# Kernel tuning notes

Measured on AMD Instinct MI355X. Metric: run time of the kernel, lower is better.

## Reference

```python
import jax, jax.numpy as jnp
import numpy as np

N = 30000
E = 480000
D_IN = 128
EPS = 1e-5
NEG_SLOPE = 0.2
# (in_dim, out_channels, heads) per GATConv layer; concat=True everywhere (PyG default)
CFG = [(D_IN, 100, 5), (500, 50, 5), (250, 32, 4), (128, 8, 4), (32, 1, 1)]
BN_DIMS = (500, 250, 128)


def setup_inputs() -> dict:
    key = jax.random.key(0)
    ks = iter(jax.random.split(key, 80))
    inp = {
        "x": jax.random.normal(next(ks), (N, D_IN), jnp.float32),
        "edge_index": jax.random.randint(next(ks), (2, E), 0, N),
        "edge_weight": jax.random.uniform(next(ks), (E, 1), jnp.float32),
    }
    for l, (cin, cout, h) in enumerate(CFG, 1):
        s = 1.0 / np.sqrt(cin)
        inp[f"W{l}"] = jax.random.normal(next(ks), (cin, h * cout), jnp.float32) * s
        inp[f"a_s{l}"] = jax.random.normal(next(ks), (1, h, cout), jnp.float32) * 0.1
        inp[f"a_d{l}"] = jax.random.normal(next(ks), (1, h, cout), jnp.float32) * 0.1
        inp[f"We{l}"] = jax.random.normal(next(ks), (1, h * cout), jnp.float32)
        inp[f"a_e{l}"] = jax.random.normal(next(ks), (1, h, cout), jnp.float32) * 0.1
        inp[f"b{l}"] = jnp.zeros((h * cout,), jnp.float32)
    for l, d in zip((1, 2, 3), BN_DIMS):
        inp[f"g{l}"] = jnp.ones((d,), jnp.float32)
        inp[f"beta{l}"] = jnp.zeros((d,), jnp.float32)
    return inp


def _gat(x, src, dst, ea, W, a_s, a_d, We, a_e, b, heads, cout):
    """PyG GATConv with edge_dim attention (concat=True)."""
    n = x.shape[0]
    h = (x @ W).reshape(n, heads, cout)            # [N,H,C]
    e = (ea @ We).reshape(-1, heads, cout)         # [E,H,C]
    al_src = (h * a_s).sum(-1)                     # [N,H]
    al_dst = (h * a_d).sum(-1)                     # [N,H]
    logit = jax.nn.leaky_relu(al_src[src] + al_dst[dst] + (e * a_e).sum(-1), NEG_SLOPE)
    m = jax.ops.segment_max(logit, dst, num_segments=n)
    m = jnp.where(jnp.isfinite(m), m, 0.0)
    ex = jnp.exp(logit - m[dst])                   # [E,H]
    den = jax.ops.segment_sum(ex, dst, num_segments=n)
    alpha = ex / jnp.maximum(den[dst], 1e-16)      # segment softmax over in-edges of dst
    out = jax.ops.segment_sum(h[src] * alpha[..., None], dst, num_segments=n)
    return out.reshape(n, heads * cout) + b


def _bn(x, g, b):
    mu = x.mean(0)
    var = x.var(0)  # biased, as torch uses for normalization
    return (x - mu) * jax.lax.rsqrt(var + EPS) * g + b


def reference(x, edge_index, edge_weight,
              W1, a_s1, a_d1, We1, a_e1, b1,
              W2, a_s2, a_d2, We2, a_e2, b2,
              W3, a_s3, a_d3, We3, a_e3, b3,
              W4, a_s4, a_d4, We4, a_e4, b4,
              W5, a_s5, a_d5, We5, a_e5, b5,
              g1, beta1, g2, beta2, g3, beta3):
    # add self loops (PyG default) with edge_attr fill_value='mean'
    loop = jnp.arange(N)
    src = jnp.concatenate([edge_index[0], loop])
    dst = jnp.concatenate([edge_index[1], loop])
    ea = jnp.concatenate([edge_weight, jnp.full((N, 1), edge_weight.mean(), edge_weight.dtype)], axis=0)

    h = _gat(x, src, dst, ea, W1, a_s1, a_d1, We1, a_e1, b1, 5, 100)
    h = jax.nn.relu(_bn(h, g1, beta1))
    h = _gat(h, src, dst, ea, W2, a_s2, a_d2, We2, a_e2, b2, 5, 50)
    h = jax.nn.relu(_bn(h, g2, beta2))
    h = _gat(h, src, dst, ea, W3, a_s3, a_d3, We3, a_e3, b3, 4, 32)
    h = jax.nn.relu(_bn(h, g3, beta3))
    h = _gat(h, src, dst, ea, W4, a_s4, a_d4, We4, a_e4, b4, 4, 8)
    h = jax.nn.relu(h)
    h = _gat(h, src, dst, ea, W5, a_s5, a_d5, We5, a_e5, b5, 1, 1)
    return h
```

## Files before the change

### kernel.cpp

```cpp
#include <hip/hip_runtime.h>
#include <hip/hip_bf16.h>
#include <math.h>

#define NN 30000
#define EE 480000
#define ET (EE + NN)
#define NEG_SLOPE 0.2f
#define BN_EPS 1e-5f

struct LayerCfg { int cin, C, H; };
static const LayerCfg g_cfg[5] = {
    {128, 100, 5}, {500, 50, 5}, {250, 32, 4}, {128, 8, 4}, {32, 1, 1}
};

typedef short short8 __attribute__((ext_vector_type(8)));
typedef float f32x4 __attribute__((ext_vector_type(4)));

__device__ __forceinline__ unsigned short f2bf(float f) {
    unsigned int u = __builtin_bit_cast(unsigned int, f);
    u = (u + 0x7FFFu + ((u >> 16) & 1u)) >> 16;
    return (unsigned short)u;
}
__device__ __forceinline__ float bf2f(unsigned short h) {
    unsigned int u = ((unsigned int)h) << 16;
    return __builtin_bit_cast(float, u);
}


struct PrepArgs {
    const float* W[5];
    const float* We[5];
    const float* ae[5];
    unsigned short* bh[5];
    unsigned short* bl[5];
    float* wedot;
    int K[5], N[5], Kp[5], Np[5], C[5], H[5];
};

static const int EBLK = (ET + 255) / 256;

__global__ void prep_fused_kernel(const int* __restrict__ ei, int* __restrict__ rank,
                                  int* __restrict__ cnt, const float* __restrict__ ew,
                                  float* __restrict__ esum, PrepArgs a) {
    __shared__ float sdata[256];
    __shared__ float tile[32][33];
    int b = blockIdx.x;
    int tid = threadIdx.x;

    if (b < EBLK) {
        int e = b * 256 + tid;
        if (e < ET) {
            int d = (e < EE) ? ei[EE + e] : (e - EE);
            rank[e] = atomicAdd(&cnt[d], 1);
        }
        return;
    }
    b -= EBLK;
    if (b < 256) {
        float s = 0.f;
        for (int i = b * 256 + tid; i < EE; i += 65536)
            s += ew[i];
        sdata[tid] = s;
        __syncthreads();
        for (int off = 128; off > 0; off >>= 1) {
            if (tid < off) sdata[tid] += sdata[tid + off];
            __syncthreads();
        }
        if (tid == 0) atomicAdd(esum, sdata[0]);
        return;
    }
    b -= 256;
    int bx = b & 15, by = (b >> 4) & 15, bz = b >> 8;
    int l = bz;
    int tx = tid & 31, ty = tid >> 5;
    if (bx == 0 && by == 0 && ty == 0 && tx < 8) {
        int hd = tx;
        if (hd < a.H[l]) {
            int C = a.C[l];
            const float* We = a.We[l] + hd * C;
            const float* ae = a.ae[l] + hd * C;
            float s = 0.f;
            for (int c = 0; c < C; c++) s += We[c] * ae[c];
            a.wedot[l * 8 + hd] = s;
        }
    }
    int Kp = a.Kp[l], Np = a.Np[l], K = a.K[l], N = a.N[l];
    int kb = bx * 32, nb = by * 32;
    if (kb >= Kp || nb >= Np) return;
    const float* B = a.W[l];
    unsigned short* Bth = a.bh[l];
    unsigned short* Btl = a.bl[l];
#pragma unroll
    for (int i = 0; i < 4; i++) {
        int k = kb + ty + i * 8, n = nb + tx;
        tile[ty + i * 8][tx] = (k < K && n < N) ? B[(size_t)k * N + n] : 0.f;
    }
    __syncthreads();
#pragma unroll
    for (int i = 0; i < 4; i++) {
        int n = nb + ty + i * 8, k = kb + tx;
        if (n < Np && k < Kp) {
            float v = tile[tx][ty + i * 8];
            unsigned short hi = f2bf(v);
            unsigned short lo = f2bf(v - bf2f(hi));
            size_t idx = (size_t)n * Kp + k;
            Bth[idx] = hi;
            Btl[idx] = lo;
        }
    }
}

__global__ void scan_kernel(const int* __restrict__ cnt, int* __restrict__ off) {
    __shared__ int lsum[1024];
    const int T = 1024;
    int t = threadIdx.x;
    int chunk = (NN + T - 1) / T;
    int base = t * chunk;
    int end = min(NN, base + chunk);
    int s = 0;
    for (int i = base; i < end; i++) s += cnt[i];
    lsum[t] = s;
    __syncthreads();
    for (int d = 1; d < T; d <<= 1) {
        int v = (t >= d) ? lsum[t - d] : 0;
        __syncthreads();
        lsum[t] += v;
        __syncthreads();
    }
    int run = (t == 0) ? 0 : lsum[t - 1];
    for (int i = base; i < end; i++) {
        off[i] = run;
        run += cnt[i];
    }
    if (t == 0) off[NN] = ET;
}

__global__ void fill_kernel(const int* __restrict__ ei, const int* __restrict__ rank,
                            const float* __restrict__ ew, const float* __restrict__ esum,
                            const int* __restrict__ off,
                            int* __restrict__ csr_src, float* __restrict__ csr_ea) {
    int e = blockIdx.x * blockDim.x + threadIdx.x;
    if (e >= ET) return;
    int sv, d;
    if (e < EE) { sv = ei[e]; d = ei[EE + e]; }
    else        { sv = e - EE; d = e - EE; }
    int p = off[d] + rank[e];
    csr_src[p] = sv;
    csr_ea[p]  = (e < EE) ? ew[e] : esum[0] * (1.0f / (float)EE);
}

#define GBM 128
#define GBNT 128
#define GBK 32
#define ASTR 36
__global__ __launch_bounds__(256) void gemm_split_kernel(const float* __restrict__ A,
                                                         const unsigned short* __restrict__ Bt_hi,
                                                         const unsigned short* __restrict__ Bt_lo,
                                                         float* __restrict__ Cm,
                                                         unsigned short* __restrict__ Ch16,
                                                         int M, int Kp, int Nc,
                                                         const float* __restrict__ colsum,
                                                         const float* __restrict__ colsumsq,
                                                         const float* __restrict__ g,
                                                         const float* __restrict__ beta,
                                                         int D) {
    __shared__ short AsH[GBM * ASTR];
    __shared__ short AsL[GBM * ASTR];
    __shared__ short BsH[GBNT * ASTR];
    __shared__ short BsL[GBNT * ASTR];
    __shared__ float sscale[512];
    __shared__ float sshift[512];
    int tid = threadIdx.x;
    bool bn = (colsum != nullptr);
    if (bn) {
        for (int c = tid; c < Kp; c += 256) {
            float sc = 0.f, sh = 0.f;
            if (c < D) {
                float mu = colsum[c] * (1.0f / (float)NN);
                float var = colsumsq[c] * (1.0f / (float)NN) - mu * mu;
                sc = g[c] * rsqrtf(var + BN_EPS);
                sh = beta[c] - mu * sc;
            }
            sscale[c] = sc;
            sshift[c] = sh;
        }
        __syncthreads();
    }
    int wave = tid >> 6, lane = tid & 63;
    int q = lane >> 4, r = lane & 15;
    int m0 = blockIdx.y * GBM, n0 = blockIdx.x * GBNT;
    int wm = (wave & 1) * 64, wn = (wave >> 1) * 64;
    f32x4 acc[4][4];
#pragma unroll
    for (int i = 0; i < 4; i++)
#pragma unroll
        for (int j = 0; j < 4; j++) acc[i][j] = (f32x4)(0.f);

    int arow2 = tid >> 1;
    int acol2 = (tid & 1) * 16;
    int brow = tid >> 2;
    int bcol = (tid & 3) * 8;

    int ksteps = Kp / GBK;
    for (int ks = 0; ks < ksteps; ks++) {
        int k0 = ks * GBK;
        {
            int m = m0 + arow2;
            float v[16];
            if (m < M) {
                const float* Ap = A + (size_t)m * Kp + k0 + acol2;
                float4 f0 = *(const float4*)(Ap);
                float4 f1 = *(const float4*)(Ap + 4);
                float4 f2 = *(const float4*)(Ap + 8);
                float4 f3 = *(const float4*)(Ap + 12);
                v[0]=f0.x; v[1]=f0.y; v[2]=f0.z; v[3]=f0.w;
                v[4]=f1.x; v[5]=f1.y; v[6]=f1.z; v[7]=f1.w;
                v[8]=f2.x; v[9]=f2.y; v[10]=f2.z; v[11]=f2.w;
                v[12]=f3.x; v[13]=f3.y; v[14]=f3.z; v[15]=f3.w;
                if (bn) {
                    int cb = k0 + acol2;
#pragma unroll
                    for (int i = 0; i < 16; i++)
                        v[i] = fmaxf(v[i] * sscale[cb + i] + sshift[cb + i], 0.f);
                }
            } else {
#pragma unroll
                for (int i = 0; i < 16; i++) v[i] = 0.f;
            }
#pragma unroll
            for (int i = 0; i < 16; i++) {
                unsigned short hi = f2bf(v[i]);
                unsigned short lo = f2bf(v[i] - bf2f(hi));
                AsH[arow2 * ASTR + acol2 + i] = (short)hi;
                AsL[arow2 * ASTR + acol2 + i] = (short)lo;
            }
        }
#pragma unroll
        for (int p = 0; p < 2; p++) {
            int row = p * 64 + brow;
            size_t gidx = (size_t)(n0 + row) * Kp + k0 + bcol;
            *((uint4*)(BsH + row * ASTR + bcol)) = *((const uint4*)(Bt_hi + gidx));
            *((uint4*)(BsL + row * ASTR + bcol)) = *((const uint4*)(Bt_lo + gidx));
        }
        __syncthreads();
        short8 ah[4], al[4], bh[4], bl[4];
#pragma unroll
        for (int i = 0; i < 4; i++) {
            ah[i] = *((const short8*)(AsH + (wm + i * 16 + r) * ASTR + q * 8));
            al[i] = *((const short8*)(AsL + (wm + i * 16 + r) * ASTR + q * 8));
        }
#pragma unroll
        for (int j = 0; j < 4; j++) {
            bh[j] = *((const short8*)(BsH + (wn + j * 16 + r) * ASTR + q * 8));
            bl[j] = *((const short8*)(BsL + (wn + j * 16 + r) * ASTR + q * 8));
        }
#pragma unroll
        for (int i = 0; i < 4; i++)
#pragma unroll
            for (int j = 0; j < 4; j++) {
                acc[i][j] = __builtin_amdgcn_mfma_f32_16x16x32_bf16(ah[i], bh[j], acc[i][j], 0, 0, 0);
                acc[i][j] = __builtin_amdgcn_mfma_f32_16x16x32_bf16(ah[i], bl[j], acc[i][j], 0, 0, 0);
                acc[i][j] = __builtin_amdgcn_mfma_f32_16x16x32_bf16(al[i], bh[j], acc[i][j], 0, 0, 0);
            }
        __syncthreads();
    }
#pragma unroll
    for (int i = 0; i < 4; i++) {
#pragma unroll
        for (int j = 0; j < 4; j++) {
#pragma unroll
            for (int reg = 0; reg < 4; reg++) {
                int mrow = m0 + wm + i * 16 + q * 4 + reg;
                int ncol = n0 + wn + j * 16 + r;
                if (mrow < M && ncol < Nc) {
                    float val = acc[i][j][reg];
                    if (Cm)   Cm[(size_t)mrow * Nc + ncol] = val;
                    if (Ch16) Ch16[(size_t)mrow * Nc + ncol] = f2bf(val);
                }
            }
        }
    }
}

__global__ void gemv_l5_kernel(const float* __restrict__ X, const float* __restrict__ W,
                               const float* __restrict__ a_s, const float* __restrict__ a_d,
                               float* __restrict__ h, float* __restrict__ al_src,
                               float* __restrict__ al_dst) {
    __shared__ float w[32];
    if (threadIdx.x < 32) w[threadIdx.x] = W[threadIdx.x];
    __syncthreads();
    int n = blockIdx.x * blockDim.x + threadIdx.x;
    if (n >= NN) return;
    const float* row = X + (size_t)n * 32;
    float s = 0.f;
#pragma unroll
    for (int i = 0; i < 8; i++) {
        float4 f = *(const float4*)(row + i * 4);
        s += f.x * w[i * 4] + f.y * w[i * 4 + 1] + f.z * w[i * 4 + 2] + f.w * w[i * 4 + 3];
    }
    h[n] = s;
    al_src[n] = s * a_s[0];
    al_dst[n] = s * a_d[0];
}

__global__ void al_wave_h16_kernel(const unsigned short* __restrict__ h16,
                                   const float* __restrict__ a_s,
                                   const float* __restrict__ a_d,
                                   float* __restrict__ al_src, float* __restrict__ al_dst,
                                   int H, int C, int HCp) {
    int w = (blockIdx.x * blockDim.x + threadIdx.x) >> 6;
    int lane = threadIdx.x & 63;
    if (w >= NN) return;
    const unsigned short* row = h16 + (size_t)w * HCp;
    float s1[5] = {0.f, 0.f, 0.f, 0.f, 0.f};
    float s2[5] = {0.f, 0.f, 0.f, 0.f, 0.f};
#pragma unroll
    for (int hd = 0; hd < 5; hd++) {
        if (hd >= H) break;
        int base = hd * C;
        for (int c = lane * 2; c < C; c += 128) {
            unsigned int u = *(const unsigned int*)(row + base + c);
            float v0 = bf2f((unsigned short)(u & 0xffffu));
            float v1 = bf2f((unsigned short)(u >> 16));
            s1[hd] += v0 * a_s[base + c] + v1 * a_s[base + c + 1];
            s2[hd] += v0 * a_d[base + c] + v1 * a_d[base + c + 1];
        }
    }
#pragma unroll
    for (int hd = 0; hd < 5; hd++) {
        if (hd >= H) break;
#pragma unroll
        for (int off = 32; off > 0; off >>= 1) {
            s1[hd] += __shfl_xor(s1[hd], off, 64);
            s2[hd] += __shfl_xor(s2[hd], off, 64);
        }
    }
    if (lane == 0) {
#pragma unroll
        for (int hd = 0; hd < 5; hd++) {
            if (hd >= H) break;
            al_src[(size_t)w * H + hd] = s1[hd];
            al_dst[(size_t)w * H + hd] = s2[hd];
        }
    }
}

__global__ void attn_kernel(const float* __restrict__ al_src,
                            const float* __restrict__ al_dst,
                            const int* __restrict__ csr_src,
                            const float* __restrict__ csr_ea,
                            const float* __restrict__ we_dot,
                            const int* __restrict__ off,
                            float* __restrict__ alpha_t, int H, int NH) {
    int t = blockIdx.x * blockDim.x + threadIdx.x;
    if (t >= NH) return;
    int n = t / H, hd = t - n * H;
    int s = off[n], e = off[n + 1];
    float ad = al_dst[(size_t)n * H + hd];
    float wd = we_dot[hd];
    float* arow = alpha_t + (size_t)hd * ET;
    float m = -INFINITY, l = 0.f;
    int p = s;
    for (; p + 3 < e; p += 4) {
        int s0 = csr_src[p], s1 = csr_src[p + 1], s2 = csr_src[p + 2], s3 = csr_src[p + 3];
        float w0 = csr_ea[p], w1 = csr_ea[p + 1], w2 = csr_ea[p + 2], w3 = csr_ea[p + 3];
        float l0 = al_src[(size_t)s0 * H + hd] + ad + w0 * wd;
        float l1 = al_src[(size_t)s1 * H + hd] + ad + w1 * wd;
        float l2 = al_src[(size_t)s2 * H + hd] + ad + w2 * wd;
        float l3 = al_src[(size_t)s3 * H + hd] + ad + w3 * wd;
        l0 = (l0 >= 0.f) ? l0 : NEG_SLOPE * l0;
        l1 = (l1 >= 0.f) ? l1 : NEG_SLOPE * l1;
        l2 = (l2 >= 0.f) ? l2 : NEG_SLOPE * l2;
        l3 = (l3 >= 0.f) ? l3 : NEG_SLOPE * l3;
        arow[p] = l0; arow[p + 1] = l1; arow[p + 2] = l2; arow[p + 3] = l3;
        float mq = fmaxf(fmaxf(l0, l1), fmaxf(l2, l3));
        float nm = fmaxf(m, mq);
        l = l * __expf(m - nm)
          + __expf(l0 - nm) + __expf(l1 - nm) + __expf(l2 - nm) + __expf(l3 - nm);
        m = nm;
    }
    for (; p < e; p++) {
        float lg = al_src[(size_t)csr_src[p] * H + hd] + ad + csr_ea[p] * wd;
        lg = (lg >= 0.f) ? lg : NEG_SLOPE * lg;
        arow[p] = lg;
        float nm = fmaxf(m, lg);
        l = l * __expf(m - nm) + __expf(lg - nm);
        m = nm;
    }
    float inv = 1.f / fmaxf(l, 1e-16f);
    for (p = s; p < e; p++) arow[p] = __expf(arow[p] - m) * inv;
}

__global__ void aggregate_slab_kernel(const unsigned short* __restrict__ h16,
                                      const float* __restrict__ alpha_t,
                                      const int* __restrict__ off,
                                      const int* __restrict__ csr_src,
                                      const float* __restrict__ bias,
                                      float* __restrict__ out,
                                      int C, int H, int HC, int hp,
                                      int lns, int lcps, int npr,
                                      int relu, int opitch) {
    int vs = blockIdx.x & 7;
    int nb = blockIdx.x >> 3;
    int slab = vs & ((1 << lns) - 1);
    int rep  = vs >> lns;
    int tid = threadIdx.x;
    int cps = 1 << lcps;
    int lc = tid & (cps - 1);
    int ln = tid >> lcps;
    int npb = 256 >> lcps;
    int nl = nb * npb + ln;
    if (nl >= npr) return;
    int n = rep * npr + nl;
    int j = (slab << (lcps + 2)) + (lc << 2);

    int hdA = j / C;
    int hdB = (j + 3) / C;
    int bnd = (hdA + 1) * C - j;
    bnd = (bnd > 4) ? 4 : bnd;
    float mA = (hdA < H) ? 1.f : 0.f;
    float mB = (hdB < H) ? 1.f : 0.f;
    const float* arA = alpha_t + (size_t)((hdA < H) ? hdA : 0) * ET;
    const float* arB = alpha_t + (size_t)((hdB < H) ? hdB : 0) * ET;

    int s = off[n], e = off[n + 1];
    const unsigned short* hb = h16 + j;
    float ac0 = 0.f, ac1 = 0.f, ac2 = 0.f, ac3 = 0.f;
    int p = s;
    for (; p + 3 < e; p += 4) {
        int idx[4]; float aA[4], aB[4];
#pragma unroll
        for (int u = 0; u < 4; u++) {
            idx[u] = csr_src[p + u];
            aA[u] = arA[p + u];
            aB[u] = arB[p + u];
        }
#pragma unroll
        for (int u = 0; u < 4; u++) {
            ushort4 uv = *(const ushort4*)(hb + (size_t)idx[u] * hp);
            ac0 += ((0 < bnd) ? aA[u] : aB[u]) * bf2f(uv.x);
            ac1 += ((1 < bnd) ? aA[u] : aB[u]) * bf2f(uv.y);
            ac2 += ((2 < bnd) ? aA[u] : aB[u]) * bf2f(uv.z);
            ac3 += ((3 < bnd) ? aA[u] : aB[u]) * bf2f(uv.w);
        }
    }
    for (; p < e; p++) {
        int i0 = csr_src[p];
        float aA0 = arA[p], aB0 = arB[p];
        ushort4 uv = *(const ushort4*)(hb + (size_t)i0 * hp);
        ac0 += ((0 < bnd) ? aA0 : aB0) * bf2f(uv.x);
        ac1 += ((1 < bnd) ? aA0 : aB0) * bf2f(uv.y);
        ac2 += ((2 < bnd) ? aA0 : aB0) * bf2f(uv.z);
        ac3 += ((3 < bnd) ? aA0 : aB0) * bf2f(uv.w);
    }
    float o0 = ac0 * ((0 < bnd) ? mA : mB) + ((j + 0 < HC) ? bias[j + 0] : 0.f);
    float o1 = ac1 * ((1 < bnd) ? mA : mB) + ((j + 1 < HC) ? bias[j + 1] : 0.f);
    float o2 = ac2 * ((2 < bnd) ? mA : mB) + ((j + 2 < HC) ? bias[j + 2] : 0.f);
    float o3 = ac3 * ((3 < bnd) ? mA : mB) + ((j + 3 < HC) ? bias[j + 3] : 0.f);
    if (relu) {
        o0 = fmaxf(o0, 0.f); o1 = fmaxf(o1, 0.f);
        o2 = fmaxf(o2, 0.f); o3 = fmaxf(o3, 0.f);
    }
    *(float4*)(out + (size_t)n * opitch + j) = make_float4(o0, o1, o2, o3);
}

__global__ void aggregate_kernel(const float* __restrict__ hfeat,
                                 const float* __restrict__ alpha_t,
                                 const int* __restrict__ off, const int* __restrict__ csr_src,
                                 const float* __restrict__ bias, float* __restrict__ out,
                                 int total) {
    int t = blockIdx.x * blockDim.x + threadIdx.x;
    if (t >= total) return;
    int n = t;
    int s = off[n], e = off[n + 1];
    float acc = 0.f;
    int p = s;
    for (; p + 3 < e; p += 4) {
        acc += alpha_t[p] * hfeat[csr_src[p]]
             + alpha_t[p + 1] * hfeat[csr_src[p + 1]]
             + alpha_t[p + 2] * hfeat[csr_src[p + 2]]
             + alpha_t[p + 3] * hfeat[csr_src[p + 3]];
    }
    for (; p < e; p++) acc += alpha_t[p] * hfeat[csr_src[p]];
    out[n] = acc + bias[0];
}


__global__ void bn_stats_kernel(const float* __restrict__ x, float* __restrict__ colsum,
                                float* __restrict__ colsumsq, int D, int pitch) {
    int rows_per_block = (NN + gridDim.x - 1) / gridDim.x;
    int r0 = blockIdx.x * rows_per_block;
    int r1 = min(NN, r0 + rows_per_block);
    int c0 = threadIdx.x;
    int c1 = threadIdx.x + 256;
    float s0 = 0.f, q0 = 0.f, s1 = 0.f, q1 = 0.f;
    for (int r = r0; r < r1; r++) {
        const float* row = x + (size_t)r * pitch;
        if (c0 < D) { float v = row[c0]; s0 += v; q0 += v * v; }
        if (c1 < D) { float v = row[c1]; s1 += v; q1 += v * v; }
    }
    if (c0 < D) { atomicAdd(&colsum[c0], s0); atomicAdd(&colsumsq[c0], q0); }
    if (c1 < D) { atomicAdd(&colsum[c1], s1); atomicAdd(&colsumsq[c1], q1); }
}


static inline size_t align_up(size_t v, size_t a) { return (v + a - 1) / a * a; }

extern "C" void kernel_launch(void* const* d_in, const int* in_sizes, int n_in,
                              void* d_out, int out_size, void* d_ws, size_t ws_size,
                              hipStream_t stream) {
    const float* x_in = (const float*)d_in[0];
    const int* ei     = (const int*)d_in[1];
    const float* ew   = (const float*)d_in[2];

    char* pws = (char*)d_ws;
    size_t off_b = 0;
    auto alloc = [&](size_t bytes) -> void* {
        void* rp = pws + off_b;
        off_b = align_up(off_b + bytes, 256);
        return rp;
    };
    float* B0      = (float*)alloc((size_t)NN * 4);
    float* B1      = (float*)alloc((size_t)NN * 512 * 4);
    unsigned short* H16 = (unsigned short*)alloc((size_t)NN * 512 * 2);
    float* alpha_t = (float*)alloc((size_t)ET * 5 * 4);
    unsigned short* Wt_hi = (unsigned short*)alloc((size_t)600 * 512 * 2);
    unsigned short* Wt_lo = (unsigned short*)alloc((size_t)600 * 512 * 2);
    float* al_src  = (float*)alloc((size_t)NN * 5 * 4);
    float* al_dst  = (float*)alloc((size_t)NN * 5 * 4);
    float* csr_ea  = (float*)alloc((size_t)ET * 4);
    int* rankb     = (int*)alloc((size_t)ET * 4);
    int* csr_src   = (int*)alloc((size_t)ET * 4);
    int* offarr    = (int*)alloc((size_t)(NN + 1) * 4);
    float* we_dot  = (float*)alloc(40 * 4);
    float* esum    = (float*)alloc(4);
    int* cnt       = (int*)alloc((size_t)NN * 4);
    float* colsum_all   = (float*)alloc(3 * 512 * 4);
    float* colsumsq_all = (float*)alloc(3 * 512 * 4);
    char* zero_end = pws + off_b;
    (void)ws_size; (void)n_in; (void)in_sizes; (void)out_size;

    int Kp[5], Np[5], hp[5];
    size_t wtoff[5];
    size_t acc_off = 0;
    for (int l = 0; l < 5; l++) {
        int K = g_cfg[l].cin, HC = g_cfg[l].C * g_cfg[l].H;
        Kp[l] = (K + 31) / 32 * 32;
        Np[l] = (HC + 127) / 128 * 128;
        hp[l] = (HC >= 64) ? ((HC + 63) / 64 * 64) : ((HC + 7) / 8 * 8);
        wtoff[l] = acc_off;
        acc_off += (size_t)Kp[l] * Np[l];
    }

    PrepArgs pa;
    for (int l = 0; l < 5; l++) {
        pa.W[l]  = (const float*)d_in[3 + l * 6 + 0];
        pa.We[l] = (const float*)d_in[3 + l * 6 + 3];
        pa.ae[l] = (const float*)d_in[3 + l * 6 + 4];
        pa.bh[l] = Wt_hi + wtoff[l];
        pa.bl[l] = Wt_lo + wtoff[l];
        pa.K[l] = g_cfg[l].cin;
        pa.N[l] = g_cfg[l].C * g_cfg[l].H;
        pa.Kp[l] = Kp[l];
        pa.Np[l] = Np[l];
        pa.C[l] = g_cfg[l].C;
        pa.H[l] = g_cfg[l].H;
    }
    pa.wedot = we_dot;

    hipMemsetAsync(esum, 0, (size_t)(zero_end - (char*)esum), stream);
    int ebl = EBLK;
    prep_fused_kernel<<<ebl + 256 + 1280, 256, 0, stream>>>(ei, rankb, cnt, ew, esum, pa);
    scan_kernel<<<1, 1024, 0, stream>>>(cnt, offarr);
    fill_kernel<<<ebl, 256, 0, stream>>>(ei, rankb, ew, esum, offarr, csr_src, csr_ea);

    for (int l = 0; l < 5; l++) {
        const LayerCfg& cf = g_cfg[l];
        int H = cf.H, C = cf.C;
        int HC = H * C;
        const float* a_s = (const float*)d_in[3 + l * 6 + 1];
        const float* a_d = (const float*)d_in[3 + l * 6 + 2];
        const float* b   = (const float*)d_in[3 + l * 6 + 5];

        const float* X = (l == 0) ? x_in : B1;
        float* outbuf = (l == 4) ? (float*)d_out : B1;
        int opitch = (l == 4) ? 1 : Kp[l + 1];
        int NH = NN * H;
        int alblocks = (NN * 64 + 255) / 256;

        if (l == 4) {
            gemv_l5_kernel<<<(NN + 255) / 256, 256, 0, stream>>>(
                X, pa.W[4], a_s, a_d, B0, al_src, al_dst);
        } else {
            const float* cs = (l >= 1) ? colsum_all + (l - 1) * 512 : nullptr;
            const float* cq = (l >= 1) ? colsumsq_all + (l - 1) * 512 : nullptr;
            const float* gg = (l >= 1) ? (const float*)d_in[33 + (l - 1) * 2 + 0] : nullptr;
            const float* bb = (l >= 1) ? (const float*)d_in[33 + (l - 1) * 2 + 1] : nullptr;
            int Din = (l >= 1) ? g_cfg[l - 1].C * g_cfg[l - 1].H : 0;
            dim3 ggrid(Np[l] / GBNT, (NN + GBM - 1) / GBM);
            gemm_split_kernel<<<ggrid, 256, 0, stream>>>(X, Wt_hi + wtoff[l], Wt_lo + wtoff[l],
                                                         nullptr, H16,
                                                         NN, Kp[l], hp[l], cs, cq, gg, bb, Din);
            al_wave_h16_kernel<<<alblocks, 256, 0, stream>>>(H16, a_s, a_d, al_src, al_dst, H, C, hp[l]);
        }

        attn_kernel<<<(NH + 255) / 256, 256, 0, stream>>>(al_src, al_dst, csr_src, csr_ea,
                                                          we_dot + l * 8, offarr, alpha_t, H, NH);

        if (l == 4) {
            aggregate_kernel<<<(NN + 255) / 256, 256, 0, stream>>>(
                B0, alpha_t, offarr, csr_src, b, outbuf, NN);
        } else {
            int cps = (hp[l] >= 64) ? 16 : 8;
            int lcps = (cps == 16) ? 4 : 3;
            int nslabs = hp[l] / (cps * 4);
            int lns = (nslabs == 8) ? 3 : (nslabs == 4) ? 2 : (nslabs == 2) ? 1 : 0;
            int dup = 8 / nslabs;
            int npr = NN / dup;
            int npb = 256 / cps;
            int gx = 8 * ((npr + npb - 1) / npb);
            aggregate_slab_kernel<<<gx, 256, 0, stream>>>(
                H16, alpha_t, offarr, csr_src, b, outbuf,
                C, H, HC, hp[l], lns, lcps, npr, (l == 3) ? 1 : 0, opitch);
        }

        if (l < 3) {
            bn_stats_kernel<<<512, 256, 0, stream>>>(outbuf, colsum_all + l * 512,
                                                     colsumsq_all + l * 512, HC, opitch);
        }
    }
}
```

Measured before the change: 821.3 us.

## Stage neighbor indices and attention weights in LDS for slab aggregation

```diff
diff --git a/kernel.cpp b/kernel.cpp
--- a/kernel.cpp
+++ b/kernel.cpp
@@ -391,72 +391,122 @@
     for (p = s; p < e; p++) arow[p] = __expf(arow[p] - m) * inv;
 }
 
-__global__ void aggregate_slab_kernel(const unsigned short* __restrict__ h16,
-                                      const float* __restrict__ alpha_t,
-                                      const int* __restrict__ off,
-                                      const int* __restrict__ csr_src,
-                                      const float* __restrict__ bias,
-                                      float* __restrict__ out,
-                                      int C, int H, int HC, int hp,
-                                      int lns, int lcps, int npr,
-                                      int relu, int opitch) {
+#define AGG_T 64
+__global__ void aggregate_slab_lds_kernel(const unsigned short* __restrict__ h16,
+                                          const float* __restrict__ alpha_t,
+                                          const int* __restrict__ off,
+                                          const int* __restrict__ csr_src,
+                                          const float* __restrict__ bias,
+                                          float* __restrict__ out,
+                                          int C, int H, int HC, int hp,
+                                          int lns, int lcps, int npr, int nhs,
+                                          int relu, int opitch) {
+    extern __shared__ char smem[];
+    int cps = 1 << lcps;
+    int G = 256 >> lcps;
+    int* sidx = (int*)smem;
+    float* sal = (float*)(smem + (size_t)G * AGG_T * 4);
+    __shared__ int s_maxt;
+
     int vs = blockIdx.x & 7;
     int nb = blockIdx.x >> 3;
     int slab = vs & ((1 << lns) - 1);
     int rep  = vs >> lns;
     int tid = threadIdx.x;
-    int cps = 1 << lcps;
     int lc = tid & (cps - 1);
-    int ln = tid >> lcps;
-    int npb = 256 >> lcps;
-    int nl = nb * npb + ln;
-    if (nl >= npr) return;
-    int n = rep * npr + nl;
-    int j = (slab << (lcps + 2)) + (lc << 2);
+    int g = tid >> lcps;
+    int nl = nb * G + g;
+    bool active = (nl < npr);
+    int n = rep * npr + (active ? nl : 0);
+
+    int slab_j = slab << (lcps + 2);
+    int j = slab_j + (lc << 2);
+    int hlo = slab_j / C;
+    int hhi = (slab_j + (cps << 2) - 1) / C;
+    if (hhi > H - 1) hhi = H - 1;
+    int nval = hhi - hlo + 1;
 
     int hdA = j / C;
     int hdB = (j + 3) / C;
     int bnd = (hdA + 1) * C - j;
     bnd = (bnd > 4) ? 4 : bnd;
-    float mA = (hdA < H) ? 1.f : 0.f;
-    float mB = (hdB < H) ? 1.f : 0.f;
-    const float* arA = alpha_t + (size_t)((hdA < H) ? hdA : 0) * ET;
-    const float* arB = alpha_t + (size_t)((hdB < H) ? hdB : 0) * ET;
-
-    int s = off[n], e = off[n + 1];
+    int selA = hdA - hlo; if (selA >= nhs) selA = nhs - 1;
+    int selB = hdB - hlo; if (selB >= nhs) selB = nhs - 1;
+
+    int s = active ? off[n] : 0;
+    int e = active ? off[n + 1] : 0;
+    int nt = (e - s + AGG_T - 1) / AGG_T;
+
+    if (tid == 0) s_maxt = 0;
+    __syncthreads();
+    if (lc == 0 && active && nt > 0) atomicMax(&s_maxt, nt);
+    __syncthreads();
+    int maxt = s_maxt;
+
     const unsigned short* hb = h16 + j;
+    int* myidx = sidx + g * AGG_T;
+    float* myal = sal + (size_t)g * nhs * AGG_T;
     float ac0 = 0.f, ac1 = 0.f, ac2 = 0.f, ac3 = 0.f;
-    int p = s;
-    for (; p + 3 < e; p += 4) {
-        int idx[4]; float aA[4], aB[4];
-#pragma unroll
-        for (int u = 0; u < 4; u++) {
-            idx[u] = csr_src[p + u];
-            aA[u] = arA[p + u];
-            aB[u] = arB[p + u];
-        }
-#pragma unroll
-        for (int u = 0; u < 4; u++) {
-            ushort4 uv = *(const ushort4*)(hb + (size_t)idx[u] * hp);
-            ac0 += ((0 < bnd) ? aA[u] : aB[u]) * bf2f(uv.x);
-            ac1 += ((1 < bnd) ? aA[u] : aB[u]) * bf2f(uv.y);
-            ac2 += ((2 < bnd) ? aA[u] : aB[u]) * bf2f(uv.z);
-            ac3 += ((3 < bnd) ? aA[u] : aB[u]) * bf2f(uv.w);
-        }
-    }
-    for (; p < e; p++) {
-        int i0 = csr_src[p];
-        float aA0 = arA[p], aB0 = arB[p];
-        ushort4 uv = *(const ushort4*)(hb + (size_t)i0 * hp);
-        ac0 += ((0 < bnd) ? aA0 : aB0) * bf2f(uv.x);
-        ac1 += ((1 < bnd) ? aA0 : aB0) * bf2f(uv.y);
-        ac2 += ((2 < bnd) ? aA0 : aB0) * bf2f(uv.z);
-        ac3 += ((3 < bnd) ? aA0 : aB0) * bf2f(uv.w);
-    }
-    float o0 = ac0 * ((0 < bnd) ? mA : mB) + ((j + 0 < HC) ? bias[j + 0] : 0.f);
-    float o1 = ac1 * ((1 < bnd) ? mA : mB) + ((j + 1 < HC) ? bias[j + 1] : 0.f);
-    float o2 = ac2 * ((2 < bnd) ? mA : mB) + ((j + 2 < HC) ? bias[j + 2] : 0.f);
-    float o3 = ac3 * ((3 < bnd) ? mA : mB) + ((j + 3 < HC) ? bias[j + 3] : 0.f);
+
+    for (int t = 0; t < maxt; t++) {
+        int base = s + t * AGG_T;
+        int cnt = e - base;
+        if (cnt < 0) cnt = 0;
+        if (cnt > AGG_T) cnt = AGG_T;
+        __syncthreads();
+        for (int q = lc; q < AGG_T; q += cps)
+            myidx[q] = (q < cnt) ? csr_src[base + q] : 0;
+        for (int r = 0; r < nhs; r++) {
+            bool hv = (r < nval);
+            const float* ar = alpha_t + (size_t)(hlo + r) * ET;
+            float* dst = myal + r * AGG_T;
+            for (int q = lc; q < AGG_T; q += cps)
+                dst[q] = (hv && q < cnt) ? ar[base + q] : 0.f;
+        }
+        __syncthreads();
+        const float* aA = myal + selA * AGG_T;
+        const float* aB = myal + selB * AGG_T;
+        int q = 0;
+        for (; q + 3 < cnt; q += 4) {
+            int i0 = myidx[q], i1 = myidx[q + 1], i2 = myidx[q + 2], i3 = myidx[q + 3];
+            float a0 = aA[q], a1 = aA[q + 1], a2 = aA[q + 2], a3 = aA[q + 3];
+            float b0 = aB[q], b1 = aB[q + 1], b2 = aB[q + 2], b3 = aB[q + 3];
+            ushort4 u0 = *(const ushort4*)(hb + (size_t)i0 * hp);
+            ushort4 u1 = *(const ushort4*)(hb + (size_t)i1 * hp);
+            ushort4 u2 = *(const ushort4*)(hb + (size_t)i2 * hp);
+            ushort4 u3 = *(const ushort4*)(hb + (size_t)i3 * hp);
+            ac0 += ((0 < bnd) ? a0 : b0) * bf2f(u0.x);
+            ac1 += ((1 < bnd) ? a0 : b0) * bf2f(u0.y);
+            ac2 += ((2 < bnd) ? a0 : b0) * bf2f(u0.z);
+            ac3 += ((3 < bnd) ? a0 : b0) * bf2f(u0.w);
+            ac0 += ((0 < bnd) ? a1 : b1) * bf2f(u1.x);
+            ac1 += ((1 < bnd) ? a1 : b1) * bf2f(u1.y);
+            ac2 += ((2 < bnd) ? a1 : b1) * bf2f(u1.z);
+            ac3 += ((3 < bnd) ? a1 : b1) * bf2f(u1.w);
+            ac0 += ((0 < bnd) ? a2 : b2) * bf2f(u2.x);
+            ac1 += ((1 < bnd) ? a2 : b2) * bf2f(u2.y);
+            ac2 += ((2 < bnd) ? a2 : b2) * bf2f(u2.z);
+            ac3 += ((3 < bnd) ? a2 : b2) * bf2f(u2.w);
+            ac0 += ((0 < bnd) ? a3 : b3) * bf2f(u3.x);
+            ac1 += ((1 < bnd) ? a3 : b3) * bf2f(u3.y);
+            ac2 += ((2 < bnd) ? a3 : b3) * bf2f(u3.z);
+            ac3 += ((3 < bnd) ? a3 : b3) * bf2f(u3.w);
+        }
+        for (; q < cnt; q++) {
+            int i0 = myidx[q];
+            float a0 = aA[q], b0 = aB[q];
+            ushort4 uv = *(const ushort4*)(hb + (size_t)i0 * hp);
+            ac0 += ((0 < bnd) ? a0 : b0) * bf2f(uv.x);
+            ac1 += ((1 < bnd) ? a0 : b0) * bf2f(uv.y);
+            ac2 += ((2 < bnd) ? a0 : b0) * bf2f(uv.z);
+            ac3 += ((3 < bnd) ? a0 : b0) * bf2f(uv.w);
+        }
+    }
+    if (!active) return;
+    float o0 = ac0 + ((j + 0 < HC) ? bias[j + 0] : 0.f);
+    float o1 = ac1 + ((j + 1 < HC) ? bias[j + 1] : 0.f);
+    float o2 = ac2 + ((j + 2 < HC) ? bias[j + 2] : 0.f);
+    float o3 = ac3 + ((j + 3 < HC) ? bias[j + 3] : 0.f);
     if (relu) {
         o0 = fmaxf(o0, 0.f); o1 = fmaxf(o1, 0.f);
         o2 = fmaxf(o2, 0.f); o3 = fmaxf(o3, 0.f);
@@ -613,15 +663,23 @@
         } else {
             int cps = (hp[l] >= 64) ? 16 : 8;
             int lcps = (cps == 16) ? 4 : 3;
-            int nslabs = hp[l] / (cps * 4);
+            int slabcols = cps * 4;
+            int nslabs = hp[l] / slabcols;
             int lns = (nslabs == 8) ? 3 : (nslabs == 4) ? 2 : (nslabs == 2) ? 1 : 0;
             int dup = 8 / nslabs;
             int npr = NN / dup;
-            int npb = 256 / cps;
-            int gx = 8 * ((npr + npb - 1) / npb);
-            aggregate_slab_kernel<<<gx, 256, 0, stream>>>(
+            int G = 256 / cps;
+            int gx = 8 * ((npr + G - 1) / G);
+            int nhs = 1;
+            for (int sbi = 0; sbi < nslabs; sbi++) {
+                int j0 = sbi * slabcols;
+                int span = (j0 + slabcols - 1) / C - j0 / C + 1;
+                if (span > nhs) nhs = span;
+            }
+            size_t smem = (size_t)G * AGG_T * 4 + (size_t)G * nhs * AGG_T * 4;
+            aggregate_slab_lds_kernel<<<gx, 256, smem, stream>>>(
                 H16, alpha_t, offarr, csr_src, b, outbuf,
-                C, H, HC, hp[l], lns, lcps, npr, (l == 3) ? 1 : 0, opitch);
+                C, H, HC, hp[l], lns, lcps, npr, nhs, (l == 3) ? 1 : 0, opitch);
         }
 
         if (l < 3) {
```

Measured after the change: 826.3 us. No clear change (+0.6%).
